# Performance work log

Hardware: AMD Instinct MI355X
Metric: run time of the kernel (lower is better)

The kernel has to match this reference:

```python
import jax, jax.numpy as jnp
import numpy as np

B, D = 32768, 512
ANCHOR_CLASS = 0  # module starts with self.a = 0; labels guarantee >1 sample of class 0


def setup_inputs() -> dict:
    key = jax.random.key(0)
    k0, k1, k2, k3, k4 = jax.random.split(key, 5)
    return {
        "label": jax.random.randint(k0, (B,), 0, 7, dtype=jnp.int64),
        "p_t": jax.random.normal(k1, (B, D), dtype=jnp.float32),
        "p_a": jax.random.normal(k2, (B, D), dtype=jnp.float32),
        "s_t": jax.random.normal(k3, (B, D), dtype=jnp.float32),
        "s_a": jax.random.normal(k4, (B, D), dtype=jnp.float32),
    }


def _modality_loss(X, anchor_idx, pos_mask, neg_mask):
    # cosine similarity of every row vs. the anchor row, fully vectorized
    anchor = X[anchor_idx]                                 # [D]
    dots = X @ anchor                                      # [B]
    cos = dots / (jnp.linalg.norm(X, axis=1) * jnp.linalg.norm(anchor))
    pos_cnt = jnp.sum(pos_mask)
    neg_cnt = jnp.sum(neg_mask)
    pos_score = jnp.where(pos_cnt > 0,
                          jnp.sum(jnp.where(pos_mask, cos, 0.0)) / jnp.maximum(pos_cnt, 1),
                          0.0)
    neg_score = jnp.where(neg_cnt > 0,
                          jnp.sum(jnp.where(neg_mask, cos, 0.0)) / jnp.maximum(neg_cnt, 1),
                          0.0)
    return 2.0 - pos_score + neg_score


def reference(label, p_t, p_a, s_t, s_a):
    a = ANCHOR_CLASS
    is_class = (label == a)
    # deterministic anchor: first sample of the anchor class (original draws one
    # uniformly; any member gives the same math structure)
    anchor_idx = jnp.argmax(is_class)
    not_anchor = jnp.arange(label.shape[0]) != anchor_idx
    pos_mask = is_class & not_anchor
    neg_mask = (~is_class) & not_anchor

    losses = jnp.stack([
        _modality_loss(p_t, anchor_idx, pos_mask, neg_mask),
        _modality_loss(p_a, anchor_idx, pos_mask, neg_mask),
        _modality_loss(s_t, anchor_idx, pos_mask, neg_mask),
        _modality_loss(s_a, anchor_idx, pos_mask, neg_mask),
    ])
    return jnp.mean(losses)
```

## Files before the change

kernel.cpp:

```cpp
#include <hip/hip_runtime.h>
#include <cstdint>

#define B_ROWS   32768
#define D_DIM    512
#define NBLOCKS  512
#define TPB      256
#define WPB      (TPB / 64)
#define NWAVES   (NBLOCKS * WPB)
#define RPW      (B_ROWS / NWAVES)

struct Ws {
    unsigned anchor_idx;
    int      cnt0;
};

#define WAITVM(N) do { asm volatile("s_waitcnt vmcnt(" #N ")" ::: "memory"); \
                       __builtin_amdgcn_sched_barrier(0); } while (0)

typedef __attribute__((address_space(3))) unsigned int lds_u32;
typedef const __attribute__((address_space(1))) unsigned int glb_u32;

__device__ __forceinline__ void dma1k(const float* src, const float4* dst) {
    __builtin_amdgcn_global_load_lds((glb_u32*)(uintptr_t)src,
                                     (lds_u32*)(unsigned int)(uintptr_t)dst,
                                     16, 0, 0);
}

__device__ __forceinline__ void dma_row(const float* const X[4], unsigned r,
                                        const float4* dstbase, int lane) {
    #pragma unroll
    for (int m = 0; m < 4; ++m) {
        const float* src = X[m] + (size_t)r * D_DIM + lane * 4;
        dma1k(src,       dstbase + m * 128);
        dma1k(src + 256, dstbase + m * 128 + 64);
    }
}

__device__ __forceinline__ float dot4(float4 a, float4 b) {
    return a.x * b.x + a.y * b.y + a.z * b.z + a.w * b.w;
}

__device__ __forceinline__ float fold_reduce8(const float v[8], int lane) {
    float w[4];
    #pragma unroll
    for (int i = 0; i < 4; ++i) {
        float send = (lane & 32) ? v[i] : v[i + 4];
        float rcv  = __shfl_xor(send, 32);
        w[i] = ((lane & 32) ? v[i + 4] : v[i]) + rcv;
    }
    float u[2];
    #pragma unroll
    for (int i = 0; i < 2; ++i) {
        float send = (lane & 16) ? w[i] : w[i + 2];
        float rcv  = __shfl_xor(send, 16);
        u[i] = ((lane & 16) ? w[i + 2] : w[i]) + rcv;
    }
    float t;
    {
        float send = (lane & 8) ? u[0] : u[1];
        float rcv  = __shfl_xor(send, 8);
        t = ((lane & 8) ? u[1] : u[0]) + rcv;
    }
    t += __shfl_xor(t, 4);
    t += __shfl_xor(t, 2);
    t += __shfl_xor(t, 1);
    return t;
}

__global__ void scan_labels_kernel(const int* __restrict__ label, Ws* ws) {
    int tid = blockIdx.x * blockDim.x + threadIdx.x;
    const int4* L4 = (const int4*)label;
    int4 v = L4[tid];
    int cnt = (v.x == 0) + (v.y == 0) + (v.z == 0) + (v.w == 0);
    unsigned base = (unsigned)tid * 4;
    unsigned mymin = 0xFFFFFFFFu;
    if (v.w == 0) mymin = base + 3;
    if (v.z == 0) mymin = base + 2;
    if (v.y == 0) mymin = base + 1;
    if (v.x == 0) mymin = base;
    for (int off = 32; off; off >>= 1) {
        cnt += __shfl_xor(cnt, off);
        unsigned o = (unsigned)__shfl_xor((int)mymin, off);
        mymin = mymin < o ? mymin : o;
    }
    if ((threadIdx.x & 63) == 0) {
        if (cnt) atomicAdd(&ws->cnt0, cnt);
        if (mymin != 0xFFFFFFFFu) atomicMin(&ws->anchor_idx, mymin);
    }
}

__launch_bounds__(TPB, 2)
__global__ void cos_accum_kernel(const int* __restrict__ label,
                                 const float* __restrict__ p_t,
                                 const float* __restrict__ p_a,
                                 const float* __restrict__ s_t,
                                 const float* __restrict__ s_a,
                                 const Ws* __restrict__ ws,
                                 float* __restrict__ partials) {
    const float* X[4] = {p_t, p_a, s_t, s_a};
    __shared__ float4 buf[WPB][2][512];
    __shared__ float  red[WPB][8];

    const unsigned aidx = ws->anchor_idx;
    const int lane = threadIdx.x & 63;
    const int wid  = __builtin_amdgcn_readfirstlane((int)(threadIdx.x >> 6));
    const unsigned gwave = (unsigned)blockIdx.x * WPB + (unsigned)wid;

    float4 an[8];
    #pragma unroll
    for (int m = 0; m < 4; ++m) {
        const float4* A = (const float4*)(X[m] + (size_t)aidx * D_DIM);
        an[2 * m]     = A[lane];
        an[2 * m + 1] = A[64 + lane];
    }
    dma_row(X, gwave,          &buf[wid][0][0], lane);
    dma_row(X, gwave + NWAVES, &buf[wid][1][0], lane);

    int lab[RPW];
    #pragma unroll
    for (int k = 0; k < RPW; ++k) lab[k] = label[gwave + (unsigned)k * NWAVES];

    float inv_mine;
    {
        float va[8];
        #pragma unroll
        for (int m = 0; m < 4; ++m) {
            va[m]     = dot4(an[2 * m], an[2 * m]) + dot4(an[2 * m + 1], an[2 * m + 1]);
            va[m + 4] = 0.f;
        }
        inv_mine = rsqrtf(fold_reduce8(va, lane));
    }

    float posAcc = 0.f, negAcc = 0.f;

    #pragma unroll
    for (int k = 0; k < RPW; ++k) {
        if (k < RPW - 1) { WAITVM(8); }
        else            { WAITVM(0); }

        const unsigned r = gwave + (unsigned)k * NWAVES;
        const float4* bp = &buf[wid][k & 1][0];

        float4 x[8];
        #pragma unroll
        for (int m = 0; m < 4; ++m) {
            x[2 * m]     = bp[m * 128 + lane];
            x[2 * m + 1] = bp[m * 128 + 64 + lane];
        }
        float v[8];
        #pragma unroll
        for (int m = 0; m < 4; ++m) {
            v[m]     = dot4(x[2 * m], an[2 * m]) + dot4(x[2 * m + 1], an[2 * m + 1]);
            v[m + 4] = dot4(x[2 * m], x[2 * m])  + dot4(x[2 * m + 1], x[2 * m + 1]);
        }

        if (k + 2 < RPW)
            dma_row(X, gwave + (unsigned)(k + 2) * NWAVES, &buf[wid][k & 1][0], lane);

        float t     = fold_reduce8(v, lane);
        float other = __shfl_xor(t, 32);
        if (((lane & 39) == 0) && (r != aidx)) {
            float c = t * rsqrtf(other) * inv_mine;
            if (lab[k] == 0) posAcc += c; else negAcc += c;
        }
    }

    if ((lane & 39) == 0) {
        int m = lane >> 3;
        red[wid][m]     = posAcc;
        red[wid][4 + m] = negAcc;
    }
    __syncthreads();
    if (threadIdx.x < 8) {
        int j = threadIdx.x;
        partials[blockIdx.x * 8 + j] = red[0][j] + red[1][j] + red[2][j] + red[3][j];
    }
}

__global__ void finalize_kernel(const Ws* __restrict__ ws,
                                const float* __restrict__ partials,
                                float* __restrict__ out) {
    __shared__ float red[256];
    int t = threadIdx.x;
    int j = t & 7;
    float s = 0.f;
    for (int r = t >> 3; r < NBLOCKS; r += 32)
        s += partials[r * 8 + j];
    red[t] = s;
    __syncthreads();
    if (t < 8) {
        float tot = 0.f;
        #pragma unroll
        for (int k = 0; k < 32; ++k) tot += red[k * 8 + t];
        red[t] = tot;
    }
    __syncthreads();
    if (t == 0) {
        float pos_cnt = (float)ws->cnt0;
        float neg_cnt = (float)(B_ROWS - (ws->cnt0 + 1));
        float total = 0.f;
        #pragma unroll
        for (int m = 0; m < 4; ++m) {
            float ps = (pos_cnt > 0.f) ? red[m]     / fmaxf(pos_cnt, 1.f) : 0.f;
            float ns = (neg_cnt > 0.f) ? red[4 + m] / fmaxf(neg_cnt, 1.f) : 0.f;
            total += 2.0f - ps + ns;
        }
        out[0] = total * 0.25f;
    }
}

extern "C" void kernel_launch(void* const* d_in, const int* in_sizes, int n_in,
                              void* d_out, int out_size, void* d_ws, size_t ws_size,
                              hipStream_t stream) {
    const int*   label = (const int*)  d_in[0];
    const float* p_t   = (const float*)d_in[1];
    const float* p_a   = (const float*)d_in[2];
    const float* s_t   = (const float*)d_in[3];
    const float* s_a   = (const float*)d_in[4];
    Ws* ws = (Ws*)d_ws;
    float* partials = (float*)d_ws + 64;

    hipMemsetAsync(d_ws, 0xFF, 8, stream);

    scan_labels_kernel <<<32,      TPB, 0, stream>>>(label, ws);
    cos_accum_kernel   <<<NBLOCKS, TPB, 0, stream>>>(label, p_t, p_a, s_t, s_a, ws, partials);
    finalize_kernel    <<<1,       TPB, 0, stream>>>(ws, partials, (float*)d_out);
}
```

Before: 61.26 us.

## Fuse finalize into main kernel, load rows to registers, early-exit anchor scan

```diff
diff --git a/kernel.cpp b/kernel.cpp
--- a/kernel.cpp
+++ b/kernel.cpp
@@ -8,36 +8,24 @@
 #define WPB      (TPB / 64)
 #define NWAVES   (NBLOCKS * WPB)
 #define RPW      (B_ROWS / NWAVES)
+#define STRIDE_B 4194304ULL
 
 struct Ws {
     unsigned anchor_idx;
-    int      cnt0;
+    int      done;
 };
+
+typedef float f32x4 __attribute__((ext_vector_type(4)));
 
 #define WAITVM(N) do { asm volatile("s_waitcnt vmcnt(" #N ")" ::: "memory"); \
                        __builtin_amdgcn_sched_barrier(0); } while (0)
 
-typedef __attribute__((address_space(3))) unsigned int lds_u32;
-typedef const __attribute__((address_space(1))) unsigned int glb_u32;
-
-__device__ __forceinline__ void dma1k(const float* src, const float4* dst) {
-    __builtin_amdgcn_global_load_lds((glb_u32*)(uintptr_t)src,
-                                     (lds_u32*)(unsigned int)(uintptr_t)dst,
-                                     16, 0, 0);
-}
-
-__device__ __forceinline__ void dma_row(const float* const X[4], unsigned r,
-                                        const float4* dstbase, int lane) {
-    #pragma unroll
-    for (int m = 0; m < 4; ++m) {
-        const float* src = X[m] + (size_t)r * D_DIM + lane * 4;
-        dma1k(src,       dstbase + m * 128);
-        dma1k(src + 256, dstbase + m * 128 + 64);
-    }
-}
-
-__device__ __forceinline__ float dot4(float4 a, float4 b) {
-    return a.x * b.x + a.y * b.y + a.z * b.z + a.w * b.w;
+__device__ __forceinline__ void ld4(f32x4& d, uint64_t a) {
+    asm volatile("global_load_dwordx4 %0, %1, off" : "=&v"(d) : "v"(a) : "memory");
+}
+
+__device__ __forceinline__ float dot4(f32x4 a, f32x4 b) {
+    return a[0] * b[0] + a[1] * b[1] + a[2] * b[2] + a[3] * b[3];
 }
 
 __device__ __forceinline__ float fold_reduce8(const float v[8], int lane) {
@@ -67,27 +55,58 @@
     return t;
 }
 
-__global__ void scan_labels_kernel(const int* __restrict__ label, Ws* ws) {
-    int tid = blockIdx.x * blockDim.x + threadIdx.x;
-    const int4* L4 = (const int4*)label;
-    int4 v = L4[tid];
-    int cnt = (v.x == 0) + (v.y == 0) + (v.z == 0) + (v.w == 0);
-    unsigned base = (unsigned)tid * 4;
-    unsigned mymin = 0xFFFFFFFFu;
-    if (v.w == 0) mymin = base + 3;
-    if (v.z == 0) mymin = base + 2;
-    if (v.y == 0) mymin = base + 1;
-    if (v.x == 0) mymin = base;
-    for (int off = 32; off; off >>= 1) {
-        cnt += __shfl_xor(cnt, off);
-        unsigned o = (unsigned)__shfl_xor((int)mymin, off);
-        mymin = mymin < o ? mymin : o;
-    }
-    if ((threadIdx.x & 63) == 0) {
-        if (cnt) atomicAdd(&ws->cnt0, cnt);
-        if (mymin != 0xFFFFFFFFu) atomicMin(&ws->anchor_idx, mymin);
-    }
-}
+__global__ void find_anchor_kernel(const int* __restrict__ label, Ws* ws) {
+    __shared__ unsigned smin[4];
+    __shared__ unsigned sres;
+    const int t = threadIdx.x, lane = t & 63, wid = t >> 6;
+    for (unsigned base = 0; base < B_ROWS; base += 1024) {
+        int4 v = ((const int4*)label)[(base >> 2) + t];
+        unsigned idx = base + (unsigned)t * 4;
+        unsigned my = 0xFFFFFFFFu;
+        if (v.w == 0) my = idx + 3;
+        if (v.z == 0) my = idx + 2;
+        if (v.y == 0) my = idx + 1;
+        if (v.x == 0) my = idx;
+        #pragma unroll
+        for (int off = 32; off; off >>= 1) {
+            unsigned o = (unsigned)__shfl_xor((int)my, off);
+            my = my < o ? my : o;
+        }
+        if (lane == 0) smin[wid] = my;
+        __syncthreads();
+        if (t == 0) {
+            unsigned m = min(min(smin[0], smin[1]), min(smin[2], smin[3]));
+            sres = m;
+            if (m != 0xFFFFFFFFu) ws->anchor_idx = m;
+        }
+        __syncthreads();
+        if (sres != 0xFFFFFFFFu) return;
+        __syncthreads();
+    }
+}
+
+#define CONSUME(BUF, K, REISSUE)                                              \
+  {                                                                           \
+    float v[8];                                                               \
+    _Pragma("unroll")                                                         \
+    for (int m = 0; m < 4; ++m) {                                             \
+      v[m]     = dot4(BUF[2*m], an[2*m])  + dot4(BUF[2*m+1], an[2*m+1]);      \
+      v[m + 4] = dot4(BUF[2*m], BUF[2*m]) + dot4(BUF[2*m+1], BUF[2*m+1]);     \
+    }                                                                         \
+    __builtin_amdgcn_sched_barrier(0);                                        \
+    if (REISSUE) {                                                            \
+      _Pragma("unroll")                                                       \
+      for (int j = 0; j < 8; ++j) { ld4(BUF[j], a[j]); a[j] += STRIDE_B; }    \
+    }                                                                         \
+    __builtin_amdgcn_sched_barrier(0);                                        \
+    float t_ = fold_reduce8(v, lane);                                         \
+    float other_ = __shfl_xor(t_, 32);                                        \
+    unsigned r_ = gwave + (unsigned)(K) * NWAVES;                             \
+    if (((lane & 39) == 0) && (r_ != aidx)) {                                 \
+      float c_ = t_ * rsqrtf(other_) * inv_mine;                              \
+      if (lab[K] == 0) posAcc += c_; else negAcc += c_;                       \
+    }                                                                         \
+  }
 
 __launch_bounds__(TPB, 2)
 __global__ void cos_accum_kernel(const int* __restrict__ label,
@@ -95,31 +114,51 @@
                                  const float* __restrict__ p_a,
                                  const float* __restrict__ s_t,
                                  const float* __restrict__ s_a,
-                                 const Ws* __restrict__ ws,
-                                 float* __restrict__ partials) {
+                                 Ws* ws,
+                                 float* __restrict__ partials,
+                                 float* __restrict__ out) {
     const float* X[4] = {p_t, p_a, s_t, s_a};
-    __shared__ float4 buf[WPB][2][512];
-    __shared__ float  red[WPB][8];
+    __shared__ float red[WPB][12];
+    __shared__ float fin[256];
+    __shared__ float colsum[9];
+    __shared__ int   slast;
 
     const unsigned aidx = ws->anchor_idx;
     const int lane = threadIdx.x & 63;
-    const int wid  = __builtin_amdgcn_readfirstlane((int)(threadIdx.x >> 6));
+    const int wid  = threadIdx.x >> 6;
     const unsigned gwave = (unsigned)blockIdx.x * WPB + (unsigned)wid;
 
-    float4 an[8];
+    uint64_t a[8];
     #pragma unroll
     for (int m = 0; m < 4; ++m) {
-        const float4* A = (const float4*)(X[m] + (size_t)aidx * D_DIM);
-        an[2 * m]     = A[lane];
-        an[2 * m + 1] = A[64 + lane];
-    }
-    dma_row(X, gwave,          &buf[wid][0][0], lane);
-    dma_row(X, gwave + NWAVES, &buf[wid][1][0], lane);
+        uint64_t base = (uint64_t)(uintptr_t)X[m]
+                      + (uint64_t)gwave * (D_DIM * 4) + (uint64_t)lane * 16;
+        a[2 * m]     = base;
+        a[2 * m + 1] = base + 1024;
+    }
+
+    f32x4 an[8], xa[8], xb[8];
+    #pragma unroll
+    for (int m = 0; m < 4; ++m) {
+        uint64_t ab = (uint64_t)(uintptr_t)X[m]
+                    + (uint64_t)aidx * (D_DIM * 4) + (uint64_t)lane * 16;
+        ld4(an[2 * m], ab);
+        ld4(an[2 * m + 1], ab + 1024);
+    }
+    #pragma unroll
+    for (int j = 0; j < 8; ++j) { ld4(xa[j], a[j]); a[j] += STRIDE_B; }
+    #pragma unroll
+    for (int j = 0; j < 8; ++j) { ld4(xb[j], a[j]); a[j] += STRIDE_B; }
 
     int lab[RPW];
     #pragma unroll
-    for (int k = 0; k < RPW; ++k) lab[k] = label[gwave + (unsigned)k * NWAVES];
-
+    for (int k = 0; k < RPW; ++k)
+        lab[k] = label[__builtin_amdgcn_readfirstlane((int)(gwave + (unsigned)k * NWAVES))];
+    int myzero = 0;
+    #pragma unroll
+    for (int k = 0; k < RPW; ++k) myzero += (lab[k] == 0);
+
+    WAITVM(16);
     float inv_mine;
     {
         float va[8];
@@ -134,35 +173,11 @@
     float posAcc = 0.f, negAcc = 0.f;
 
     #pragma unroll
-    for (int k = 0; k < RPW; ++k) {
-        if (k < RPW - 1) { WAITVM(8); }
-        else            { WAITVM(0); }
-
-        const unsigned r = gwave + (unsigned)k * NWAVES;
-        const float4* bp = &buf[wid][k & 1][0];
-
-        float4 x[8];
-        #pragma unroll
-        for (int m = 0; m < 4; ++m) {
-            x[2 * m]     = bp[m * 128 + lane];
-            x[2 * m + 1] = bp[m * 128 + 64 + lane];
-        }
-        float v[8];
-        #pragma unroll
-        for (int m = 0; m < 4; ++m) {
-            v[m]     = dot4(x[2 * m], an[2 * m]) + dot4(x[2 * m + 1], an[2 * m + 1]);
-            v[m + 4] = dot4(x[2 * m], x[2 * m])  + dot4(x[2 * m + 1], x[2 * m + 1]);
-        }
-
-        if (k + 2 < RPW)
-            dma_row(X, gwave + (unsigned)(k + 2) * NWAVES, &buf[wid][k & 1][0], lane);
-
-        float t     = fold_reduce8(v, lane);
-        float other = __shfl_xor(t, 32);
-        if (((lane & 39) == 0) && (r != aidx)) {
-            float c = t * rsqrtf(other) * inv_mine;
-            if (lab[k] == 0) posAcc += c; else negAcc += c;
-        }
+    for (int kk = 0; kk < RPW; kk += 2) {
+        WAITVM(8);
+        CONSUME(xa, kk, (kk + 2 < RPW));
+        if (kk + 2 < RPW) { WAITVM(8); } else { WAITVM(0); }
+        CONSUME(xb, kk + 1, (kk + 3 < RPW));
     }
 
     if ((lane & 39) == 0) {
@@ -170,42 +185,54 @@
         red[wid][m]     = posAcc;
         red[wid][4 + m] = negAcc;
     }
+    if (lane == 0) red[wid][8] = (float)myzero;
     __syncthreads();
-    if (threadIdx.x < 8) {
+    if (threadIdx.x < 9) {
         int j = threadIdx.x;
-        partials[blockIdx.x * 8 + j] = red[0][j] + red[1][j] + red[2][j] + red[3][j];
-    }
-}
-
-__global__ void finalize_kernel(const Ws* __restrict__ ws,
-                                const float* __restrict__ partials,
-                                float* __restrict__ out) {
-    __shared__ float red[256];
-    int t = threadIdx.x;
-    int j = t & 7;
-    float s = 0.f;
-    for (int r = t >> 3; r < NBLOCKS; r += 32)
-        s += partials[r * 8 + j];
-    red[t] = s;
+        partials[blockIdx.x * 12 + j] = red[0][j] + red[1][j] + red[2][j] + red[3][j];
+    }
+
+    __threadfence();
     __syncthreads();
-    if (t < 8) {
-        float tot = 0.f;
-        #pragma unroll
-        for (int k = 0; k < 32; ++k) tot += red[k * 8 + t];
-        red[t] = tot;
+    if (threadIdx.x == 0) {
+        int old = atomicAdd(&ws->done, 1);
+        slast = (old == (int)(NBLOCKS - 2));
     }
     __syncthreads();
-    if (t == 0) {
-        float pos_cnt = (float)ws->cnt0;
-        float neg_cnt = (float)(B_ROWS - (ws->cnt0 + 1));
-        float total = 0.f;
-        #pragma unroll
-        for (int m = 0; m < 4; ++m) {
-            float ps = (pos_cnt > 0.f) ? red[m]     / fmaxf(pos_cnt, 1.f) : 0.f;
-            float ns = (neg_cnt > 0.f) ? red[4 + m] / fmaxf(neg_cnt, 1.f) : 0.f;
-            total += 2.0f - ps + ns;
-        }
-        out[0] = total * 0.25f;
+    if (!slast) return;
+
+    {
+        const int t = threadIdx.x;
+        int j = t >> 4;
+        int g = t & 15;
+        float s = 0.f;
+        if (j < 9) {
+            for (int r2 = g; r2 < NBLOCKS; r2 += 16)
+                s += __hip_atomic_load(&partials[r2 * 12 + j],
+                                       __ATOMIC_RELAXED, __HIP_MEMORY_SCOPE_AGENT);
+        }
+        fin[t] = s;
+        __syncthreads();
+        if (t < 9) {
+            float tot = 0.f;
+            #pragma unroll
+            for (int g2 = 0; g2 < 16; ++g2) tot += fin[t * 16 + g2];
+            colsum[t] = tot;
+        }
+        __syncthreads();
+        if (t == 0) {
+            float cnt0    = colsum[8];
+            float pos_cnt = cnt0 - 1.0f;
+            float neg_cnt = (float)B_ROWS - cnt0;
+            float total = 0.f;
+            #pragma unroll
+            for (int m = 0; m < 4; ++m) {
+                float ps = (pos_cnt > 0.f) ? colsum[m]     / fmaxf(pos_cnt, 1.f) : 0.f;
+                float ns = (neg_cnt > 0.f) ? colsum[4 + m] / fmaxf(neg_cnt, 1.f) : 0.f;
+                total += 2.0f - ps + ns;
+            }
+            out[0] = total * 0.25f;
+        }
     }
 }
 
@@ -222,7 +249,7 @@
 
     hipMemsetAsync(d_ws, 0xFF, 8, stream);
 
-    scan_labels_kernel <<<32,      TPB, 0, stream>>>(label, ws);
-    cos_accum_kernel   <<<NBLOCKS, TPB, 0, stream>>>(label, p_t, p_a, s_t, s_a, ws, partials);
-    finalize_kernel    <<<1,       TPB, 0, stream>>>(ws, partials, (float*)d_out);
-}
+    find_anchor_kernel <<<1,       TPB, 0, stream>>>(label, ws);
+    cos_accum_kernel   <<<NBLOCKS, TPB, 0, stream>>>(label, p_t, p_a, s_t, s_a,
+                                                     ws, partials, (float*)d_out);
+}
```

Measured after the change: 109.8 us. +79.2%, slower.
